# Kernel tuning notes

Hardware: AMD Instinct MI355X
Metric: run time of the kernel (lower is better)

Reference implementation:

```python
import jax, jax.numpy as jnp
import numpy as np
from jax import lax

B_, L_, H_, P_ = 4, 8192, 1024, 64  # batch, seq, d_model, d_state//4
EPS = 1e-5


def setup_inputs() -> dict:
    key = jax.random.key(0)
    ks = jax.random.split(key, 20)
    s = 1.0 / np.sqrt(H_)
    inp = {
        "zH": jax.random.normal(ks[0], (B_, L_, H_), jnp.float32),
        "zL": jax.random.normal(ks[1], (B_, L_, H_), jnp.float32),
        "x": jax.random.normal(ks[2], (B_, L_, H_), jnp.float32),
        "t": jax.random.normal(ks[3], (B_, H_), jnp.float32),
        # AdaLN projections (d_model -> 2*d_model)
        "W_projH": jax.random.normal(ks[4], (H_, 2 * H_), jnp.float32) * s,
        "b_projH": jnp.zeros((2 * H_,), jnp.float32),
        "W_projL": jax.random.normal(ks[5], (H_, 2 * H_), jnp.float32) * s,
        "b_projL": jnp.zeros((2 * H_,), jnp.float32),
        # inj Linear (3*d_model -> d_model)
        "W_inj": jax.random.normal(ks[6], (3 * H_, H_), jnp.float32) * (1.0 / np.sqrt(3 * H_)),
        "b_inj": jnp.zeros((H_,), jnp.float32),
        # S5Dual params (diagonal complex SSM, bidirectional)
        "Lambda_re": -(0.1 + 0.4 * jax.random.uniform(ks[7], (P_,), jnp.float32)),
        "Lambda_im": jnp.pi * jnp.arange(P_, dtype=jnp.float32),
        "B_re": jax.random.normal(ks[8], (P_, H_), jnp.float32) * s,
        "B_im": jax.random.normal(ks[9], (P_, H_), jnp.float32) * s,
        "Cf_re": jax.random.normal(ks[10], (H_, P_), jnp.float32) * (1.0 / np.sqrt(P_)),
        "Cf_im": jax.random.normal(ks[11], (H_, P_), jnp.float32) * (1.0 / np.sqrt(P_)),
        "Cb_re": jax.random.normal(ks[12], (H_, P_), jnp.float32) * (1.0 / np.sqrt(P_)),
        "Cb_im": jax.random.normal(ks[13], (H_, P_), jnp.float32) * (1.0 / np.sqrt(P_)),
        "D": jax.random.normal(ks[14], (H_,), jnp.float32),
        "log_dt": jnp.log(0.001) + (jnp.log(0.1) - jnp.log(0.001)) * jax.random.uniform(ks[15], (P_,), jnp.float32),
    }
    return inp


def _adaln(x, cond, W, b):
    # x: [B,L,H], cond: [B,H]
    scale, shift = jnp.split(cond @ W + b, 2, axis=-1)
    mu = jnp.mean(x, axis=-1, keepdims=True)
    var = jnp.var(x, axis=-1, keepdims=True)
    xn = (x - mu) * lax.rsqrt(var + EPS)
    return xn * (1.0 + scale[:, None, :]) + shift[:, None, :]


def _binop(e1, e2):
    a1, b1 = e1
    a2, b2 = e2
    return a1 * a2, a2 * b1 + b2


def _s5_dual(u, Lambda_re, Lambda_im, B_re, B_im, Cf_re, Cf_im, Cb_re, Cb_im, D, log_dt):
    # u: [B,L,H] real -> [B,L,H] real. Bidirectional diagonal SSM (S5 style).
    Lam = Lambda_re + 1j * Lambda_im            # [P]
    dt = jnp.exp(log_dt)                        # [P]
    Lam_bar = jnp.exp(Lam * dt)                 # [P] ZOH discretization
    Bm = B_re + 1j * B_im                       # [P,H]
    B_bar = ((Lam_bar - 1.0) / Lam)[:, None] * Bm
    Bu = jnp.einsum('blh,ph->blp', u.astype(jnp.complex64), B_bar)  # [B,L,P]
    A = jnp.broadcast_to(Lam_bar, Bu.shape)
    xs_f = lax.associative_scan(_binop, (A, Bu), axis=1)[1]
    xs_b = jnp.flip(lax.associative_scan(_binop, (A, jnp.flip(Bu, axis=1)), axis=1)[1], axis=1)
    Cf = Cf_re + 1j * Cf_im
    Cb = Cb_re + 1j * Cb_im
    y = 2.0 * jnp.einsum('blp,hp->blh', xs_f, Cf).real \
        + 2.0 * jnp.einsum('blp,hp->blh', xs_b, Cb).real \
        + D * u
    return y


def reference(zH, zL, x, t, W_projH, b_projH, W_projL, b_projL, W_inj, b_inj,
              Lambda_re, Lambda_im, B_re, B_im, Cf_re, Cf_im, Cb_re, Cb_im, D, log_dt):
    zH = _adaln(zH, t, W_projH, b_projH)
    zL = _adaln(zL, t, W_projL, b_projL)
    h = jnp.concatenate([zH, zL, x], axis=-1)          # [B,L,3H]
    h = h @ W_inj + b_inj                              # [B,L,H]
    return _s5_dual(h, Lambda_re, Lambda_im, B_re, B_im, Cf_re, Cf_im, Cb_re, Cb_im, D, log_dt)
```

## Files before the change

### kernel.cpp

```cpp
#include <hip/hip_runtime.h>


#define LN_EPS 1e-5f

typedef __attribute__((ext_vector_type(8))) short bf16x8;
typedef __attribute__((ext_vector_type(8))) unsigned short u16x8;
typedef __attribute__((ext_vector_type(4))) float f32x4;

__device__ __forceinline__ unsigned short f2bf(float f) {
  unsigned int u = __float_as_uint(f);
  u += 0x7fffu + ((u >> 16) & 1u);
  return (unsigned short)(u >> 16);
}
__device__ __forceinline__ float bf2f(unsigned short s) {
  return __uint_as_float(((unsigned int)s) << 16);
}

__device__ __forceinline__ void gload16(const void* g, void* l) {
  __builtin_amdgcn_global_load_lds((const __attribute__((address_space(1))) void*)g,
                                   (__attribute__((address_space(3))) void*)l, 16, 0, 0);
}

__device__ __forceinline__ void phase_bar() {
  __builtin_amdgcn_sched_barrier(0);
  asm volatile("" ::: "memory");
  __builtin_amdgcn_s_barrier();
  __builtin_amdgcn_sched_barrier(0);
}

__global__ void proj_k(const float* __restrict__ t,
                       const float* __restrict__ WH, const float* __restrict__ bH,
                       const float* __restrict__ WL, const float* __restrict__ bL,
                       float* __restrict__ cond) {
  const int idx = blockIdx.x * 256 + threadIdx.x;
  const int tensor = idx >> 11;
  const int j2 = idx & 2047;
  const float* W = tensor ? WL : WH;
  const float bv = tensor ? bL[j2] : bH[j2];
  float a0 = bv, a1 = bv, a2 = bv, a3 = bv;
  #pragma unroll 4
  for (int k = 0; k < 1024; ++k) {
    const float w = W[k * 2048 + j2];
    a0 += t[k] * w; a1 += t[1024 + k] * w; a2 += t[2048 + k] * w; a3 += t[3072 + k] * w;
  }
  const int which = j2 >> 10, j = j2 & 1023;
  float* c = cond + (size_t)((tensor * 2 + which) * 4) * 1024 + j;
  c[0] = a0; c[1024] = a1; c[2048] = a2; c[3072] = a3;
}

__global__ void prep_k(const float* __restrict__ Winj, unsigned short* __restrict__ WinjT,
                       const float* __restrict__ Lre, const float* __restrict__ Lim,
                       const float* __restrict__ logdt,
                       const float* __restrict__ Bre, const float* __restrict__ Bim,
                       unsigned short* __restrict__ WBuT,
                       const float* __restrict__ t,
                       const float* __restrict__ WH, const float* __restrict__ WL,
                       float* __restrict__ part) {
  __shared__ float tl[64][65];
  const int bid = blockIdx.x;
  const int tid = threadIdx.x;
  if (bid < 768) {
    const int kt = bid >> 4, nt = bid & 15;
    const int k0 = kt << 6, n0 = nt << 6;
    #pragma unroll
    for (int s = 0; s < 4; ++s) {
      const int i = s * 256 + tid;
      const int r = i >> 4, c4 = i & 15;
      const float4 v = *(const float4*)&Winj[(size_t)(k0 + r) * 1024 + n0 + c4 * 4];
      tl[c4 * 4 + 0][r] = v.x; tl[c4 * 4 + 1][r] = v.y;
      tl[c4 * 4 + 2][r] = v.z; tl[c4 * 4 + 3][r] = v.w;
    }
    __syncthreads();
    const int i = tid >> 2, j0 = (tid & 3) << 4;
    u16x8 w0, w1;
    #pragma unroll
    for (int q = 0; q < 8; ++q) w0[q] = f2bf(tl[i][j0 + q]);
    #pragma unroll
    for (int q = 0; q < 8; ++q) w1[q] = f2bf(tl[i][j0 + 8 + q]);
    *(u16x8*)&WinjT[(size_t)(n0 + i) * 3072 + k0 + j0] = w0;
    *(u16x8*)&WinjT[(size_t)(n0 + i) * 3072 + k0 + j0 + 8] = w1;
  } else if (bid < 1280) {
    const int idx = (bid - 768) * 256 + tid;
    const int j = idx >> 10, hh = idx & 1023;
    const int p = j >> 1, im = j & 1;
    const float lr = Lre[p], li = Lim[p];
    const float dt = expf(logdt[p]);
    const float e = expf(lr * dt);
    float sn, cs; sincosf(li * dt, &sn, &cs);
    const float ar = e * cs - 1.f, ai = e * sn;
    const float den = lr * lr + li * li;
    const float cr = (ar * lr + ai * li) / den;
    const float ci = (ai * lr - ar * li) / den;
    const float br = Bre[p * 1024 + hh], bi = Bim[p * 1024 + hh];
    const float v = im ? (cr * bi + ci * br) : (cr * br - ci * bi);
    WBuT[idx] = f2bf(v);
  } else {
    const int pb = bid - 1280;
    const int tensor = pb >> 7, ks = (pb >> 3) & 15, jc = pb & 7;
    const int j2 = jc * 256 + tid;
    const float* W = tensor ? WL : WH;
    float a0 = 0.f, a1 = 0.f, a2 = 0.f, a3 = 0.f;
    const int k0 = ks * 64;
    #pragma unroll 4
    for (int k = k0; k < k0 + 64; ++k) {
      const float w = W[k * 2048 + j2];
      a0 += t[k] * w; a1 += t[1024 + k] * w; a2 += t[2048 + k] * w; a3 += t[3072 + k] * w;
    }
    float* p = part + ((size_t)(tensor * 16 + ks) * 4) * 2048 + j2;
    p[0] = a0; p[2048] = a1; p[4096] = a2; p[6144] = a3;
  }
}

__global__ void proj_red_k(const float* __restrict__ part,
                           const float* __restrict__ bH, const float* __restrict__ bL,
                           float* __restrict__ cond) {
  const int idx = blockIdx.x * 256 + threadIdx.x;
  const int tensor = idx >> 13, b = (idx >> 11) & 3, j2 = idx & 2047;
  float s = tensor ? bL[j2] : bH[j2];
  #pragma unroll
  for (int ks = 0; ks < 16; ++ks)
    s += part[((size_t)(tensor * 16 + ks) * 4 + b) * 2048 + j2];
  const int which = j2 >> 10, j = j2 & 1023;
  cond[((size_t)(tensor * 2 + which) * 4 + b) * 1024 + j] = s;
}

__global__ void transpose_winj(const float* __restrict__ W, unsigned short* __restrict__ WT) {
  __shared__ float tl[64][65];
  const int kt = blockIdx.x >> 4, nt = blockIdx.x & 15;
  const int k0 = kt << 6, n0 = nt << 6;
  const int tid = threadIdx.x;
  #pragma unroll
  for (int s = 0; s < 4; ++s) {
    const int i = s * 256 + tid;
    const int r = i >> 4, c4 = i & 15;
    const float4 v = *(const float4*)&W[(size_t)(k0 + r) * 1024 + n0 + c4 * 4];
    tl[c4 * 4 + 0][r] = v.x; tl[c4 * 4 + 1][r] = v.y;
    tl[c4 * 4 + 2][r] = v.z; tl[c4 * 4 + 3][r] = v.w;
  }
  __syncthreads();
  const int i = tid >> 2, j0 = (tid & 3) << 4;
  u16x8 w0, w1;
  #pragma unroll
  for (int q = 0; q < 8; ++q) w0[q] = f2bf(tl[i][j0 + q]);
  #pragma unroll
  for (int q = 0; q < 8; ++q) w1[q] = f2bf(tl[i][j0 + 8 + q]);
  *(u16x8*)&WT[(size_t)(n0 + i) * 3072 + k0 + j0] = w0;
  *(u16x8*)&WT[(size_t)(n0 + i) * 3072 + k0 + j0 + 8] = w1;
}

__global__ void wbu_k(const float* __restrict__ Lre, const float* __restrict__ Lim,
                      const float* __restrict__ logdt,
                      const float* __restrict__ Bre, const float* __restrict__ Bim,
                      unsigned short* __restrict__ WBuT) {
  const int idx = blockIdx.x * 256 + threadIdx.x;
  const int j = idx >> 10, hh = idx & 1023;
  const int p = j >> 1, im = j & 1;
  const float lr = Lre[p], li = Lim[p];
  const float dt = expf(logdt[p]);
  const float e = expf(lr * dt);
  float sn, cs; sincosf(li * dt, &sn, &cs);
  const float ar = e * cs - 1.f, ai = e * sn;
  const float den = lr * lr + li * li;
  const float cr = (ar * lr + ai * li) / den;
  const float ci = (ai * lr - ar * li) / den;
  const float br = Bre[p * 1024 + hh], bi = Bim[p * 1024 + hh];
  const float v = im ? (cr * bi + ci * br) : (cr * br - ci * bi);
  WBuT[idx] = f2bf(v);
}

__global__ void w2_k(const float* __restrict__ Cfre, const float* __restrict__ Cfim,
                     const float* __restrict__ Cbre, const float* __restrict__ Cbim,
                     unsigned short* __restrict__ W2T) {
  const int idx = blockIdx.x * 256 + threadIdx.x;
  const int h = idx >> 8, k = idx & 255;
  const int p = (k & 127) >> 1, im = k & 1, bw = k >> 7;
  const float* Cre = bw ? Cbre : Cfre;
  const float* Cim = bw ? Cbim : Cfim;
  const float v = im ? (-2.f * Cim[h * 64 + p]) : (2.f * Cre[h * 64 + p]);
  W2T[idx] = f2bf(v);
}

__global__ __launch_bounds__(256) void adaln_k(const float* __restrict__ zH,
                                               const float* __restrict__ zL,
                                               const float* __restrict__ x,
                                               const float* __restrict__ cond,
                                               unsigned short* __restrict__ znH,
                                               unsigned short* __restrict__ znL,
                                               unsigned short* __restrict__ xbf) {
  const int row = blockIdx.x;
  const int b = row >> 13;
  const int tid = threadIdx.x;
  const size_t rbase = (size_t)row * 1024;
  const float4 vH = *(const float4*)&zH[rbase + tid * 4];
  const float4 vL = *(const float4*)&zL[rbase + tid * 4];
  float sH = vH.x + vH.y + vH.z + vH.w;
  float qH = vH.x * vH.x + vH.y * vH.y + vH.z * vH.z + vH.w * vH.w;
  float sL = vL.x + vL.y + vL.z + vL.w;
  float qL = vL.x * vL.x + vL.y * vL.y + vL.z * vL.z + vL.w * vL.w;
  #pragma unroll
  for (int m = 1; m < 64; m <<= 1) {
    sH += __shfl_xor(sH, m); qH += __shfl_xor(qH, m);
    sL += __shfl_xor(sL, m); qL += __shfl_xor(qL, m);
  }
  __shared__ float red[4][4];
  const int wv = tid >> 6, ln = tid & 63;
  if (ln == 0) { red[wv][0] = sH; red[wv][1] = qH; red[wv][2] = sL; red[wv][3] = qL; }
  __syncthreads();
  sH = red[0][0] + red[1][0] + red[2][0] + red[3][0];
  qH = red[0][1] + red[1][1] + red[2][1] + red[3][1];
  sL = red[0][2] + red[1][2] + red[2][2] + red[3][2];
  qL = red[0][3] + red[1][3] + red[2][3] + red[3][3];
  const float muH = sH * (1.f / 1024.f);
  const float rsH = rsqrtf(qH * (1.f / 1024.f) - muH * muH + LN_EPS);
  const float muL = sL * (1.f / 1024.f);
  const float rsL = rsqrtf(qL * (1.f / 1024.f) - muL * muL + LN_EPS);
  const int h0 = tid * 4;
  const float4 scH = *(const float4*)&cond[(size_t)((0 * 2 + 0) * 4 + b) * 1024 + h0];
  const float4 shH = *(const float4*)&cond[(size_t)((0 * 2 + 1) * 4 + b) * 1024 + h0];
  const float4 scL = *(const float4*)&cond[(size_t)((1 * 2 + 0) * 4 + b) * 1024 + h0];
  const float4 shL = *(const float4*)&cond[(size_t)((1 * 2 + 1) * 4 + b) * 1024 + h0];
  ushort4 oH, oL;
  oH.x = f2bf((vH.x - muH) * rsH * (1.f + scH.x) + shH.x);
  oH.y = f2bf((vH.y - muH) * rsH * (1.f + scH.y) + shH.y);
  oH.z = f2bf((vH.z - muH) * rsH * (1.f + scH.z) + shH.z);
  oH.w = f2bf((vH.w - muH) * rsH * (1.f + scH.w) + shH.w);
  oL.x = f2bf((vL.x - muL) * rsL * (1.f + scL.x) + shL.x);
  oL.y = f2bf((vL.y - muL) * rsL * (1.f + scL.y) + shL.y);
  oL.z = f2bf((vL.z - muL) * rsL * (1.f + scL.z) + shL.z);
  oL.w = f2bf((vL.w - muL) * rsL * (1.f + scL.w) + shL.w);
  *(ushort4*)&znH[rbase + h0] = oH;
  *(ushort4*)&znL[rbase + h0] = oL;
  if (xbf != nullptr) {
    const float4 vx = *(const float4*)&x[rbase + h0];
    ushort4 ox;
    ox.x = f2bf(vx.x); ox.y = f2bf(vx.y); ox.z = f2bf(vx.z); ox.w = f2bf(vx.w);
    *(ushort4*)&xbf[rbase + h0] = ox;
  }
}

__global__ __launch_bounds__(512, 2) void gemm8p_k(
    const unsigned short* __restrict__ znH, const unsigned short* __restrict__ znL,
    const unsigned short* __restrict__ xbf, const unsigned short* __restrict__ WinjT,
    const float* __restrict__ binj, unsigned short* __restrict__ hout) {
  __shared__ char lds[131072];
  const int tid = threadIdx.x;
  const int ln = tid & 63;
  const int w = tid >> 6;
  const int wm = w >> 2, wn = w & 3;
  const int l15 = ln & 15, l4 = ln >> 4;
  const int swz = (blockIdx.x & 7) * 64 + (blockIdx.x >> 3);
  const int r0 = (swz >> 2) << 8, n0 = (swz & 3) << 8;
  constexpr int NT = 48;

  auto stageA = [&](int tau, int hf) {
    const int pidx = tau >> 4;
    const unsigned short* plane = pidx == 0 ? znH : (pidx == 1 ? znL : xbf);
    const int kbase = (tau & 15) << 6;
    char* dst0 = lds + (tau & 1) * 65536 + hf * 16384;
    #pragma unroll
    for (int i = 0; i < 2; ++i) {
      const int idx = i * 512 + tid;
      const int rl = idx >> 3, ps = idx & 7;
      const int ls = ps ^ (rl & 7);
      const unsigned short* src = plane + (size_t)(r0 + hf * 128 + rl) * 1024 + kbase + ls * 8;
      gload16(src, dst0 + i * 8192 + ((tid & 0x1C0) << 4));
    }
  };
  auto stageB = [&](int tau, int hf) {
    char* dst0 = lds + (tau & 1) * 65536 + 32768 + hf * 16384;
    #pragma unroll
    for (int i = 0; i < 2; ++i) {
      const int idx = i * 512 + tid;
      const int rl = idx >> 3, ps = idx & 7;
      const int ls = ps ^ (rl & 7);
      const unsigned short* src = WinjT + (size_t)(n0 + hf * 128 + rl) * 3072 + tau * 64 + ls * 8;
      gload16(src, dst0 + i * 8192 + ((tid & 0x1C0) << 4));
    }
  };
  auto ldA = [&](int tau, int m, int kk) -> bf16x8 {
    const int row = wm * 128 + m * 16 + l15;
    const int ps = (kk * 4 + l4) ^ (row & 7);
    return *(const bf16x8*)(lds + (tau & 1) * 65536 + row * 128 + ps * 16);
  };
  auto ldB = [&](int tau, int n, int kk) -> bf16x8 {
    const int row = wn * 64 + n * 16 + l15;
    const int ps = (kk * 4 + l4) ^ (row & 7);
    return *(const bf16x8*)(lds + (tau & 1) * 65536 + 32768 + row * 128 + ps * 16);
  };

  f32x4 acc[8][4];
  #pragma unroll
  for (int m = 0; m < 8; ++m)
    #pragma unroll
    for (int n = 0; n < 4; ++n)
      acc[m][n] = (f32x4){0.f, 0.f, 0.f, 0.f};

  stageA(0, 0); stageA(0, 1); stageB(0, 0); stageB(0, 1); stageA(1, 0); stageA(1, 1);
  asm volatile("s_waitcnt vmcnt(4)" ::: "memory");
  __builtin_amdgcn_s_barrier();
  __builtin_amdgcn_sched_barrier(0);

  bf16x8 t0[4], t1[4], c0[4], c1[4], b0[4], b1[4];
  #pragma unroll
  for (int m = 0; m < 4; ++m) t0[m] = ldA(0, m, 0);
  #pragma unroll
  for (int n = 0; n < 4; ++n) b0[n] = ldB(0, n, 0);

  for (int tau = 0; tau < NT; ++tau) {
    if (tau + 1 < NT) stageB(tau + 1, 0);
    phase_bar();
    __builtin_amdgcn_s_setprio(1);
    #pragma unroll
    for (int m = 0; m < 4; ++m) t1[m] = ldA(tau, 4 + m, 0);
    #pragma unroll
    for (int m = 0; m < 4; ++m) c0[m] = ldA(tau, m, 1);
    #pragma unroll
    for (int m = 0; m < 4; ++m)
      #pragma unroll
      for (int n = 0; n < 4; ++n)
        acc[m][n] = __builtin_amdgcn_mfma_f32_16x16x32_bf16(t0[m], b0[n], acc[m][n], 0, 0, 0);
    __builtin_amdgcn_s_setprio(0);
    phase_bar();
    if (tau + 1 < NT) stageB(tau + 1, 1);
    phase_bar();
    __builtin_amdgcn_s_setprio(1);
    #pragma unroll
    for (int m = 0; m < 4; ++m) c1[m] = ldA(tau, 4 + m, 1);
    #pragma unroll
    for (int n = 0; n < 4; ++n) b1[n] = ldB(tau, n, 1);
    #pragma unroll
    for (int m = 0; m < 4; ++m)
      #pragma unroll
      for (int n = 0; n < 4; ++n)
        acc[4 + m][n] = __builtin_amdgcn_mfma_f32_16x16x32_bf16(t1[m], b0[n], acc[4 + m][n], 0, 0, 0);
    __builtin_amdgcn_s_setprio(0);
    asm volatile("s_waitcnt lgkmcnt(0)" ::: "memory");
    phase_bar();
    if (tau + 2 < NT) stageA(tau + 2, 0);
    phase_bar();
    __builtin_amdgcn_s_setprio(1);
    #pragma unroll
    for (int m = 0; m < 4; ++m)
      #pragma unroll
      for (int n = 0; n < 4; ++n)
        acc[m][n] = __builtin_amdgcn_mfma_f32_16x16x32_bf16(c0[m], b1[n], acc[m][n], 0, 0, 0);
    __builtin_amdgcn_s_setprio(0);
    phase_bar();
    if (tau + 2 < NT) stageA(tau + 2, 1);
    if (tau < NT - 2) { asm volatile("s_waitcnt vmcnt(4)" ::: "memory"); }
    else              { asm volatile("s_waitcnt vmcnt(0)" ::: "memory"); }
    phase_bar();
    __builtin_amdgcn_s_setprio(1);
    if (tau + 1 < NT) {
      #pragma unroll
      for (int m = 0; m < 4; ++m) t0[m] = ldA(tau + 1, m, 0);
      #pragma unroll
      for (int n = 0; n < 4; ++n) b0[n] = ldB(tau + 1, n, 0);
    }
    #pragma unroll
    for (int m = 0; m < 4; ++m)
      #pragma unroll
      for (int n = 0; n < 4; ++n)
        acc[4 + m][n] = __builtin_amdgcn_mfma_f32_16x16x32_bf16(c1[m], b1[n], acc[4 + m][n], 0, 0, 0);
    __builtin_amdgcn_s_setprio(0);
    phase_bar();
  }

  #pragma unroll
  for (int n = 0; n < 4; ++n) {
    const int gcol = n0 + wn * 64 + n * 16 + l15;
    const float bv = binj[gcol];
    #pragma unroll
    for (int m = 0; m < 8; ++m) {
      const int grow = r0 + wm * 128 + m * 16 + l4 * 4;
      #pragma unroll
      for (int r = 0; r < 4; ++r)
        hout[(size_t)(grow + r) * 1024 + gcol] = f2bf(acc[m][n][r] + bv);
    }
  }
}

template<int KTOT, int NTOT, int CTILES, int EPI, int AMODE>
__global__ __launch_bounds__(256, 3) void gemm_k(
    const unsigned short* __restrict__ A,
    const unsigned short* __restrict__ Bm,
    const float* __restrict__ xsrc,
    const float* __restrict__ evec,
    const unsigned short* __restrict__ hbuf,
    void* __restrict__ Cout) {
  const int tid = threadIdx.x;
  const int wv = tid >> 6, ln = tid & 63;
  const int l15 = ln & 15, l4 = ln >> 4;
  const int wr = wv >> 1, wc = wv & 1;
  const int bid = blockIdx.x;
  const int rt = bid / CTILES, ct = bid % CTILES;
  const int r0 = rt << 7, n0 = ct << 7;

  __shared__ unsigned short ldsA[128 * 32];
  __shared__ unsigned short ldsB[128 * 32];

  f32x4 acc[4][4];
  #pragma unroll
  for (int i = 0; i < 4; ++i)
    #pragma unroll
    for (int j = 0; j < 4; ++j)
      acc[i][j] = (f32x4){0.f, 0.f, 0.f, 0.f};

  for (int k0 = 0; k0 < KTOT; k0 += 32) {
    __syncthreads();
    {
      const unsigned short* bb = Bm + (size_t)n0 * KTOT + k0;
      #pragma unroll
      for (int s0 = 0; s0 < 2; ++s0) {
        const int s = wv + s0 * 4;
        const int bo = (s << 10) + (ln << 4);
        const int row = bo >> 6, inb = bo & 63;
        gload16((const char*)(bb + (size_t)row * KTOT) + inb, (char*)ldsB + (s << 10));
      }
    }
    if (AMODE == 1 && k0 >= 2048) {
      const int row = tid >> 1, kf = (tid & 1) << 4;
      const float* xp = xsrc + (size_t)(r0 + row) * 1024 + (k0 - 2048) + kf;
      const float4 v0 = *(const float4*)(xp + 0);
      const float4 v1 = *(const float4*)(xp + 4);
      const float4 v2 = *(const float4*)(xp + 8);
      const float4 v3 = *(const float4*)(xp + 12);
      u16x8 w0, w1;
      w0[0] = f2bf(v0.x); w0[1] = f2bf(v0.y); w0[2] = f2bf(v0.z); w0[3] = f2bf(v0.w);
      w0[4] = f2bf(v1.x); w0[5] = f2bf(v1.y); w0[6] = f2bf(v1.z); w0[7] = f2bf(v1.w);
      w1[0] = f2bf(v2.x); w1[1] = f2bf(v2.y); w1[2] = f2bf(v2.z); w1[3] = f2bf(v2.w);
      w1[4] = f2bf(v3.x); w1[5] = f2bf(v3.y); w1[6] = f2bf(v3.z); w1[7] = f2bf(v3.w);
      *(u16x8*)&ldsA[row * 32 + kf] = w0;
      *(u16x8*)&ldsA[row * 32 + kf + 8] = w1;
    } else {
      const unsigned short* aa;
      int astr;
      if (AMODE == 0) { aa = A + (size_t)r0 * KTOT + k0; astr = KTOT; }
      else { aa = A + (size_t)(k0 >> 10) * (32768u * 1024u) + (size_t)r0 * 1024 + (k0 & 1023); astr = 1024; }
      #pragma unroll
      for (int s0 = 0; s0 < 2; ++s0) {
        const int s = wv + s0 * 4;
        const int bo = (s << 10) + (ln << 4);
        const int row = bo >> 6, inb = bo & 63;
        gload16((const char*)(aa + (size_t)row * astr) + inb, (char*)ldsA + (s << 10));
      }
    }
    __syncthreads();
    bf16x8 af[4], bfr[4];
    #pragma unroll
    for (int i = 0; i < 4; ++i)
      af[i] = *(const bf16x8*)&ldsA[(wr * 64 + i * 16 + l15) * 32 + l4 * 8];
    #pragma unroll
    for (int j = 0; j < 4; ++j)
      bfr[j] = *(const bf16x8*)&ldsB[(wc * 64 + j * 16 + l15) * 32 + l4 * 8];
    #pragma unroll
    for (int i = 0; i < 4; ++i)
      #pragma unroll
      for (int j = 0; j < 4; ++j)
        acc[i][j] = __builtin_amdgcn_mfma_f32_16x16x32_bf16(af[i], bfr[j], acc[i][j], 0, 0, 0);
  }

  #pragma unroll
  for (int j = 0; j < 4; ++j) {
    const int gcol = n0 + wc * 64 + j * 16 + l15;
    float ev = 0.f;
    if (EPI == 1 || EPI == 3) ev = evec[gcol];
    #pragma unroll
    for (int i = 0; i < 4; ++i) {
      const int gr = r0 + wr * 64 + i * 16 + l4 * 4;
      #pragma unroll
      for (int r = 0; r < 4; ++r) {
        const size_t idx = (size_t)(gr + r) * NTOT + gcol;
        const float v = acc[i][j][r];
        if (EPI == 1)      ((unsigned short*)Cout)[idx] = f2bf(v + ev);
        else if (EPI == 2) ((float*)Cout)[idx] = v;
        else               ((float*)Cout)[idx] = v + ev * bf2f(hbuf[idx]);
      }
    }
  }
}

__global__ __launch_bounds__(256) void gemm_bu_k(
    const unsigned short* __restrict__ A, const unsigned short* __restrict__ Bm,
    float* __restrict__ Bu, float* __restrict__ agg,
    const float* __restrict__ Lre, const float* __restrict__ Lim,
    const float* __restrict__ logdt,
    const float* __restrict__ Cfre, const float* __restrict__ Cfim,
    const float* __restrict__ Cbre, const float* __restrict__ Cbim,
    unsigned short* __restrict__ W2T) {
  const int tid = threadIdx.x;
  if (blockIdx.x >= 256) {
    const int idx = (blockIdx.x - 256) * 256 + tid;
    const int h = idx >> 8, k = idx & 255;
    const int p = (k & 127) >> 1, im = k & 1, bw = k >> 7;
    const float* Cre = bw ? Cbre : Cfre;
    const float* Cim = bw ? Cbim : Cfim;
    const float v = im ? (-2.f * Cim[h * 64 + p]) : (2.f * Cre[h * 64 + p]);
    W2T[idx] = f2bf(v);
    return;
  }
  __shared__ unsigned short ldsA[128 * 32];
  __shared__ unsigned short ldsB[128 * 32];
  __shared__ float cbuf[128][128];
  const int wv = tid >> 6, ln = tid & 63;
  const int l15 = ln & 15, l4 = ln >> 4;
  const int wr = wv >> 1, wc = wv & 1;
  const int r0 = blockIdx.x << 7;

  f32x4 acc[4][4];
  #pragma unroll
  for (int i = 0; i < 4; ++i)
    #pragma unroll
    for (int j = 0; j < 4; ++j)
      acc[i][j] = (f32x4){0.f, 0.f, 0.f, 0.f};

  for (int k0 = 0; k0 < 1024; k0 += 32) {
    __syncthreads();
    {
      const unsigned short* bb = Bm + k0;
      #pragma unroll
      for (int s0 = 0; s0 < 2; ++s0) {
        const int s = wv + s0 * 4;
        const int bo = (s << 10) + (ln << 4);
        const int row = bo >> 6, inb = bo & 63;
        gload16((const char*)(bb + (size_t)row * 1024) + inb, (char*)ldsB + (s << 10));
      }
    }
    {
      const unsigned short* aa = A + (size_t)r0 * 1024 + k0;
      #pragma unroll
      for (int s0 = 0; s0 < 2; ++s0) {
        const int s = wv + s0 * 4;
        const int bo = (s << 10) + (ln << 4);
        const int row = bo >> 6, inb = bo & 63;
        gload16((const char*)(aa + (size_t)row * 1024) + inb, (char*)ldsA + (s << 10));
      }
    }
    __syncthreads();
    bf16x8 af[4], bfr[4];
    #pragma unroll
    for (int i = 0; i < 4; ++i)
      af[i] = *(const bf16x8*)&ldsA[(wr * 64 + i * 16 + l15) * 32 + l4 * 8];
    #pragma unroll
    for (int j = 0; j < 4; ++j)
      bfr[j] = *(const bf16x8*)&ldsB[(wc * 64 + j * 16 + l15) * 32 + l4 * 8];
    #pragma unroll
    for (int i = 0; i < 4; ++i)
      #pragma unroll
      for (int j = 0; j < 4; ++j)
        acc[i][j] = __builtin_amdgcn_mfma_f32_16x16x32_bf16(af[i], bfr[j], acc[i][j], 0, 0, 0);
  }

  #pragma unroll
  for (int j = 0; j < 4; ++j) {
    const int lcol = wc * 64 + j * 16 + l15;
    #pragma unroll
    for (int i = 0; i < 4; ++i) {
      const int lr0 = wr * 64 + i * 16 + l4 * 4;
      #pragma unroll
      for (int r = 0; r < 4; ++r) {
        const float v = acc[i][j][r];
        Bu[(size_t)(r0 + lr0 + r) * 128 + lcol] = v;
        cbuf[lr0 + r][lcol] = v;
      }
    }
  }
  __syncthreads();
  if (wv < 2) {
    const int dir = wv, p = ln;
    const float dt = expf(logdt[p]);
    const float e = expf(Lre[p] * dt);
    float sn, cs; sincosf(Lim[p] * dt, &sn, &cs);
    const float ar = e * cs, ai = e * sn;
    float sr = 0.f, si = 0.f;
    for (int i = 0; i < 128; ++i) {
      const int off = dir ? (127 - i) : i;
      const float vr = cbuf[off][2 * p];
      const float vi = cbuf[off][2 * p + 1];
      const float nr = ar * sr - ai * si + vr;
      const float ni = ar * si + ai * sr + vi;
      sr = nr; si = ni;
    }
    const int b = r0 >> 13, ch = (r0 & 8191) >> 7;
    float* o = agg + (((size_t)dir * 4 + b) * 64 + ch) * 128 + 2 * p;
    o[0] = sr; o[1] = si;
  }
}

__global__ void scan_agg_k(const float* __restrict__ Bu, float* __restrict__ agg,
                           const float* __restrict__ Lre, const float* __restrict__ Lim,
                           const float* __restrict__ logdt) {
  const int bid = blockIdx.x;
  const int dir = bid >> 8, b = (bid >> 6) & 3, ch = bid & 63;
  const int p = threadIdx.x;
  const float dt = expf(logdt[p]);
  const float e = expf(Lre[p] * dt);
  float sn, cs; sincosf(Lim[p] * dt, &sn, &cs);
  const float ar = e * cs, ai = e * sn;
  const int l0 = ch << 7;
  const float* base = Bu + ((size_t)b * 8192 + l0) * 128 + 2 * p;
  float sr = 0.f, si = 0.f;
  for (int g = 0; g < 16; ++g) {
    float2 v[8];
    #pragma unroll
    for (int u = 0; u < 8; ++u) {
      const int i = g * 8 + u;
      const int off = dir ? (127 - i) : i;
      v[u] = *(const float2*)(base + (size_t)off * 128);
    }
    #pragma unroll
    for (int u = 0; u < 8; ++u) {
      const float nr = ar * sr - ai * si + v[u].x;
      const float ni = ar * si + ai * sr + v[u].y;
      sr = nr; si = ni;
    }
  }
  float* o = agg + (((size_t)dir * 4 + b) * 64 + ch) * 128 + 2 * p;
  o[0] = sr; o[1] = si;
}

__global__ void scan_comb_k(const float* __restrict__ agg, float* __restrict__ pre,
                            const float* __restrict__ Lre, const float* __restrict__ Lim,
                            const float* __restrict__ logdt) {
  const int dir = blockIdx.x >> 2, b = blockIdx.x & 3;
  const int p = threadIdx.x;
  const float dt = expf(logdt[p]);
  const float e = expf(Lre[p] * dt);
  float sn, cs; sincosf(Lim[p] * dt, &sn, &cs);
  float Ar = e * cs, Ai = e * sn;
  #pragma unroll
  for (int q = 0; q < 7; ++q) {
    const float nr = Ar * Ar - Ai * Ai; Ai = 2.f * Ar * Ai; Ar = nr;
  }
  const float* ab = agg + ((size_t)(dir * 4 + b) * 64) * 128 + 2 * p;
  float* pb = pre + ((size_t)(dir * 4 + b) * 64) * 128 + 2 * p;
  float sr = 0.f, si = 0.f;
  for (int g = 0; g < 8; ++g) {
    float2 v[8];
    #pragma unroll
    for (int u = 0; u < 8; ++u) {
      const int i = g * 8 + u;
      const int ch = dir ? (63 - i) : i;
      v[u] = *(const float2*)(ab + (size_t)ch * 128);
    }
    #pragma unroll
    for (int u = 0; u < 8; ++u) {
      const int i = g * 8 + u;
      const int ch = dir ? (63 - i) : i;
      pb[(size_t)ch * 128] = sr; pb[(size_t)ch * 128 + 1] = si;
      const float nr = Ar * sr - Ai * si + v[u].x;
      const float ni = Ar * si + Ai * sr + v[u].y;
      sr = nr; si = ni;
    }
  }
}

__global__ void scan_apply_k(const float* __restrict__ Bu, const float* __restrict__ pre,
                             unsigned short* __restrict__ Xcat,
                             const float* __restrict__ Lre, const float* __restrict__ Lim,
                             const float* __restrict__ logdt) {
  const int bid = blockIdx.x;
  const int dir = bid >> 8, b = (bid >> 6) & 3, ch = bid & 63;
  const int p = threadIdx.x;
  const float dt = expf(logdt[p]);
  const float e = expf(Lre[p] * dt);
  float sn, cs; sincosf(Lim[p] * dt, &sn, &cs);
  const float ar = e * cs, ai = e * sn;
  const int l0 = ch << 7;
  const float* base = Bu + ((size_t)b * 8192 + l0) * 128 + 2 * p;
  const float* pr = pre + (((size_t)dir * 4 + b) * 64 + ch) * 128 + 2 * p;
  float sr = pr[0], si = pr[1];
  unsigned short* xb = Xcat + ((size_t)b * 8192 + l0) * 256 + dir * 128 + 2 * p;
  for (int g = 0; g < 16; ++g) {
    float2 v[8];
    #pragma unroll
    for (int u = 0; u < 8; ++u) {
      const int i = g * 8 + u;
      const int off = dir ? (127 - i) : i;
      v[u] = *(const float2*)(base + (size_t)off * 128);
    }
    #pragma unroll
    for (int u = 0; u < 8; ++u) {
      const int i = g * 8 + u;
      const int off = dir ? (127 - i) : i;
      const float nr = ar * sr - ai * si + v[u].x;
      const float ni = ar * si + ai * sr + v[u].y;
      sr = nr; si = ni;
      ushort2 ov; ov.x = f2bf(sr); ov.y = f2bf(si);
      *(ushort2*)(xb + (size_t)off * 256) = ov;
    }
  }
}

__global__ void scan_apply2_k(const float* __restrict__ Bu, const float* __restrict__ agg,
                              unsigned short* __restrict__ Xcat,
                              const float* __restrict__ Lre, const float* __restrict__ Lim,
                              const float* __restrict__ logdt) {
  const int bid = blockIdx.x;
  const int dir = bid >> 8, b = (bid >> 6) & 3, ch = bid & 63;
  const int p = threadIdx.x;
  const float dt = expf(logdt[p]);
  const float e = expf(Lre[p] * dt);
  float sn, cs; sincosf(Lim[p] * dt, &sn, &cs);
  const float ar = e * cs, ai = e * sn;
  float Ar = ar, Ai = ai;
  #pragma unroll
  for (int q = 0; q < 7; ++q) {
    const float nr = Ar * Ar - Ai * Ai; Ai = 2.f * Ar * Ai; Ar = nr;
  }
  const float* ab = agg + ((size_t)(dir * 4 + b) * 64) * 128 + 2 * p;
  float sr = 0.f, si = 0.f;
  const int nk = dir ? (63 - ch) : ch;
  for (int g0 = 0; g0 < nk; g0 += 8) {
    const int gn = (nk - g0) < 8 ? (nk - g0) : 8;
    float2 v[8];
    for (int u = 0; u < gn; ++u) {
      const int i = g0 + u;
      const int k = dir ? (63 - i) : i;
      v[u] = *(const float2*)(ab + (size_t)k * 128);
    }
    for (int u = 0; u < gn; ++u) {
      const float nr = Ar * sr - Ai * si + v[u].x;
      const float ni = Ar * si + Ai * sr + v[u].y;
      sr = nr; si = ni;
    }
  }
  const int l0 = ch << 7;
  const float* base = Bu + ((size_t)b * 8192 + l0) * 128 + 2 * p;
  unsigned short* xb = Xcat + ((size_t)b * 8192 + l0) * 256 + dir * 128 + 2 * p;
  for (int g = 0; g < 16; ++g) {
    float2 v[8];
    #pragma unroll
    for (int u = 0; u < 8; ++u) {
      const int i = g * 8 + u;
      const int off = dir ? (127 - i) : i;
      v[u] = *(const float2*)(base + (size_t)off * 128);
    }
    #pragma unroll
    for (int u = 0; u < 8; ++u) {
      const int i = g * 8 + u;
      const int off = dir ? (127 - i) : i;
      const float nr = ar * sr - ai * si + v[u].x;
      const float ni = ar * si + ai * sr + v[u].y;
      sr = nr; si = ni;
      ushort2 ov; ov.x = f2bf(sr); ov.y = f2bf(si);
      *(ushort2*)(xb + (size_t)off * 256) = ov;
    }
  }
}

extern "C" void kernel_launch(void* const* d_in, const int* in_sizes, int n_in,
                              void* d_out, int out_size, void* d_ws, size_t ws_size,
                              hipStream_t stream) {
  const float* zH    = (const float*)d_in[0];
  const float* zL    = (const float*)d_in[1];
  const float* x     = (const float*)d_in[2];
  const float* t     = (const float*)d_in[3];
  const float* WpH   = (const float*)d_in[4];
  const float* bpH   = (const float*)d_in[5];
  const float* WpL   = (const float*)d_in[6];
  const float* bpL   = (const float*)d_in[7];
  const float* Winj  = (const float*)d_in[8];
  const float* binj  = (const float*)d_in[9];
  const float* Lre   = (const float*)d_in[10];
  const float* Lim   = (const float*)d_in[11];
  const float* Bre   = (const float*)d_in[12];
  const float* Bim   = (const float*)d_in[13];
  const float* Cfre  = (const float*)d_in[14];
  const float* Cfim  = (const float*)d_in[15];
  const float* Cbre  = (const float*)d_in[16];
  const float* Cbim  = (const float*)d_in[17];
  const float* Dv    = (const float*)d_in[18];
  const float* logdt = (const float*)d_in[19];

  unsigned short* znH = (unsigned short*)d_out;
  unsigned short* znL = znH + (size_t)32768 * 1024;

  const bool FAST = ws_size >= 141950976ull;
  char* ws = (char*)d_ws;

  if (FAST) {
    unsigned short* WinjT = (unsigned short*)(ws + 0);
    unsigned short* hbuf  = (unsigned short*)(ws + 6291456);
    unsigned short* WBuT  = (unsigned short*)(ws + 73400320);
    float*          cond  = (float*)(ws + 73662464);
    float*          part  = (float*)(ws + 73793536);
    char*           U     = ws + 74842112;
    unsigned short* xbf   = (unsigned short*)U;
    float*          Bu    = (float*)(U + 0);
    float*          agg   = (float*)(U + 16777216);
    unsigned short* Xcat  = (unsigned short*)(U + 17301504);
    unsigned short* W2T   = (unsigned short*)(U + 34078720);

    prep_k<<<1536, 256, 0, stream>>>(Winj, WinjT, Lre, Lim, logdt, Bre, Bim, WBuT,
                                     t, WpH, WpL, part);
    proj_red_k<<<64, 256, 0, stream>>>(part, bpH, bpL, cond);
    adaln_k<<<32768, 256, 0, stream>>>(zH, zL, x, cond, znH, znL, xbf);
    gemm8p_k<<<512, 512, 0, stream>>>(znH, znL, xbf, WinjT, binj, hbuf);
    gemm_bu_k<<<1280, 256, 0, stream>>>(hbuf, WBuT, Bu, agg, Lre, Lim, logdt,
                                        Cfre, Cfim, Cbre, Cbim, W2T);
    scan_apply2_k<<<512, 64, 0, stream>>>(Bu, agg, Xcat, Lre, Lim, logdt);
    gemm_k<256, 1024, 8, 3, 0><<<2048, 256, 0, stream>>>(Xcat, W2T, nullptr, Dv, hbuf, (float*)d_out);
  } else {
    unsigned short* WinjT = (unsigned short*)ws; ws += (size_t)1024 * 3072 * 2;
    unsigned short* hbuf  = (unsigned short*)ws; ws += (size_t)32768 * 1024 * 2;
    unsigned short* WBuT  = (unsigned short*)ws; ws += (size_t)128 * 1024 * 2;
    float*          Bu    = (float*)ws;          ws += (size_t)32768 * 128 * 4;
    float*          cond  = (float*)ws;          ws += (size_t)2 * 2 * 4 * 1024 * 4;
    float*          agg   = (float*)ws;          ws += (size_t)2 * 4 * 64 * 128 * 4;
    float*          pre   = (float*)ws;          ws += (size_t)2 * 4 * 64 * 128 * 4;
    unsigned short* Xcat  = (unsigned short*)ws; ws += (size_t)32768 * 256 * 2;
    unsigned short* W2T   = (unsigned short*)ws; ws += (size_t)1024 * 256 * 2;

    proj_k<<<16, 256, 0, stream>>>(t, WpH, bpH, WpL, bpL, cond);
    transpose_winj<<<768, 256, 0, stream>>>(Winj, WinjT);
    wbu_k<<<512, 256, 0, stream>>>(Lre, Lim, logdt, Bre, Bim, WBuT);
    w2_k<<<1024, 256, 0, stream>>>(Cfre, Cfim, Cbre, Cbim, W2T);
    adaln_k<<<32768, 256, 0, stream>>>(zH, zL, x, cond, znH, znL, nullptr);
    gemm_k<3072, 1024, 8, 1, 1><<<2048, 256, 0, stream>>>(znH, WinjT, x, binj, nullptr, hbuf);
    gemm_k<1024, 128, 1, 2, 0><<<256, 256, 0, stream>>>(hbuf, WBuT, nullptr, nullptr, nullptr, Bu);
    scan_agg_k<<<512, 64, 0, stream>>>(Bu, agg, Lre, Lim, logdt);
    scan_comb_k<<<8, 64, 0, stream>>>(agg, pre, Lre, Lim, logdt);
    scan_apply_k<<<512, 64, 0, stream>>>(Bu, pre, Xcat, Lre, Lim, logdt);
    gemm_k<256, 1024, 8, 3, 0><<<2048, 256, 0, stream>>>(Xcat, W2T, nullptr, Dv, hbuf, (float*)d_out);
  }
}
```

Before: 460.1 us.

## Double-buffer Bu GEMM loads, reorder epilogue stores, split scan into combine+apply

The Bu projection GEMM now uses double-buffered LDS tiles with async global-to-LDS prefetch of the next K slice and vmcnt waits, so loads overlap with the MFMAs. Epilogues in several GEMMs are reordered so the column index varies fastest, which should give better-coalesced stores, and the bias loads are hoisted. The fused scan_apply2 kernel, where each block redid a serial chunk-prefix over up to 63 aggregates, is replaced by a tiny scan_comb kernel that computes the prefixes once, followed by scan_apply. This adds an extra launch and doubles the LDS used by gemm_bu_k.

Measured after the change: 403.0 us (median of 2 runs). 1.14x faster.

```diff
diff --git a/kernel.cpp b/kernel.cpp
--- a/kernel.cpp
+++ b/kernel.cpp
@@ -366,16 +366,19 @@
     phase_bar();
   }
 
-  #pragma unroll
-  for (int n = 0; n < 4; ++n) {
-    const int gcol = n0 + wn * 64 + n * 16 + l15;
-    const float bv = binj[gcol];
-    #pragma unroll
-    for (int m = 0; m < 8; ++m) {
-      const int grow = r0 + wm * 128 + m * 16 + l4 * 4;
-      #pragma unroll
-      for (int r = 0; r < 4; ++r)
-        hout[(size_t)(grow + r) * 1024 + gcol] = f2bf(acc[m][n][r] + bv);
+  float bvv[4];
+  #pragma unroll
+  for (int n = 0; n < 4; ++n) bvv[n] = binj[n0 + wn * 64 + n * 16 + l15];
+  #pragma unroll
+  for (int m = 0; m < 8; ++m) {
+    #pragma unroll
+    for (int r = 0; r < 4; ++r) {
+      const int grow = r0 + wm * 128 + m * 16 + l4 * 4 + r;
+      #pragma unroll
+      for (int n = 0; n < 4; ++n) {
+        const int gcol = n0 + wn * 64 + n * 16 + l15;
+        hout[(size_t)grow * 1024 + gcol] = f2bf(acc[m][n][r] + bvv[n]);
+      }
     }
   }
 }
@@ -460,21 +463,23 @@
         acc[i][j] = __builtin_amdgcn_mfma_f32_16x16x32_bf16(af[i], bfr[j], acc[i][j], 0, 0, 0);
   }
 
-  #pragma unroll
-  for (int j = 0; j < 4; ++j) {
-    const int gcol = n0 + wc * 64 + j * 16 + l15;
-    float ev = 0.f;
-    if (EPI == 1 || EPI == 3) ev = evec[gcol];
-    #pragma unroll
-    for (int i = 0; i < 4; ++i) {
-      const int gr = r0 + wr * 64 + i * 16 + l4 * 4;
-      #pragma unroll
-      for (int r = 0; r < 4; ++r) {
-        const size_t idx = (size_t)(gr + r) * NTOT + gcol;
+  float ev[4];
+  #pragma unroll
+  for (int j = 0; j < 4; ++j)
+    ev[j] = (EPI == 1 || EPI == 3) ? evec[n0 + wc * 64 + j * 16 + l15] : 0.f;
+  #pragma unroll
+  for (int i = 0; i < 4; ++i) {
+    #pragma unroll
+    for (int r = 0; r < 4; ++r) {
+      const int gr = r0 + wr * 64 + i * 16 + l4 * 4 + r;
+      #pragma unroll
+      for (int j = 0; j < 4; ++j) {
+        const int gcol = n0 + wc * 64 + j * 16 + l15;
+        const size_t idx = (size_t)gr * NTOT + gcol;
         const float v = acc[i][j][r];
-        if (EPI == 1)      ((unsigned short*)Cout)[idx] = f2bf(v + ev);
+        if (EPI == 1)      ((unsigned short*)Cout)[idx] = f2bf(v + ev[j]);
         else if (EPI == 2) ((float*)Cout)[idx] = v;
-        else               ((float*)Cout)[idx] = v + ev * bf2f(hbuf[idx]);
+        else               ((float*)Cout)[idx] = v + ev[j] * bf2f(hbuf[idx]);
       }
     }
   }
@@ -499,14 +504,34 @@
     W2T[idx] = f2bf(v);
     return;
   }
-  __shared__ unsigned short ldsA[128 * 32];
-  __shared__ unsigned short ldsB[128 * 32];
+  __shared__ unsigned short ldsA[2][128 * 32];
+  __shared__ unsigned short ldsB[2][128 * 32];
   __shared__ float cbuf[128][128];
   const int wv = tid >> 6, ln = tid & 63;
   const int l15 = ln & 15, l4 = ln >> 4;
   const int wr = wv >> 1, wc = wv & 1;
   const int r0 = blockIdx.x << 7;
 
+  auto stg = [&](int k) {
+    const int par = k & 1;
+    const unsigned short* bb = Bm + k * 32;
+    const unsigned short* aa = A + (size_t)r0 * 1024 + k * 32;
+    #pragma unroll
+    for (int s0 = 0; s0 < 2; ++s0) {
+      const int s = wv + s0 * 4;
+      const int bo = (s << 10) + (ln << 4);
+      const int row = bo >> 6, inb = bo & 63;
+      gload16((const char*)(bb + (size_t)row * 1024) + inb, (char*)ldsB[par] + (s << 10));
+    }
+    #pragma unroll
+    for (int s0 = 0; s0 < 2; ++s0) {
+      const int s = wv + s0 * 4;
+      const int bo = (s << 10) + (ln << 4);
+      const int row = bo >> 6, inb = bo & 63;
+      gload16((const char*)(aa + (size_t)row * 1024) + inb, (char*)ldsA[par] + (s << 10));
+    }
+  };
+
   f32x4 acc[4][4];
   #pragma unroll
   for (int i = 0; i < 4; ++i)
@@ -514,54 +539,38 @@
     for (int j = 0; j < 4; ++j)
       acc[i][j] = (f32x4){0.f, 0.f, 0.f, 0.f};
 
-  for (int k0 = 0; k0 < 1024; k0 += 32) {
-    __syncthreads();
-    {
-      const unsigned short* bb = Bm + k0;
-      #pragma unroll
-      for (int s0 = 0; s0 < 2; ++s0) {
-        const int s = wv + s0 * 4;
-        const int bo = (s << 10) + (ln << 4);
-        const int row = bo >> 6, inb = bo & 63;
-        gload16((const char*)(bb + (size_t)row * 1024) + inb, (char*)ldsB + (s << 10));
-      }
-    }
-    {
-      const unsigned short* aa = A + (size_t)r0 * 1024 + k0;
-      #pragma unroll
-      for (int s0 = 0; s0 < 2; ++s0) {
-        const int s = wv + s0 * 4;
-        const int bo = (s << 10) + (ln << 4);
-        const int row = bo >> 6, inb = bo & 63;
-        gload16((const char*)(aa + (size_t)row * 1024) + inb, (char*)ldsA + (s << 10));
-      }
-    }
-    __syncthreads();
+  stg(0);
+  for (int k = 0; k < 32; ++k) {
+    const int par = k & 1;
+    if (k + 1 < 32) { stg(k + 1); asm volatile("s_waitcnt vmcnt(4)" ::: "memory"); }
+    else            { asm volatile("s_waitcnt vmcnt(0)" ::: "memory"); }
+    __builtin_amdgcn_s_barrier();
     bf16x8 af[4], bfr[4];
     #pragma unroll
     for (int i = 0; i < 4; ++i)
-      af[i] = *(const bf16x8*)&ldsA[(wr * 64 + i * 16 + l15) * 32 + l4 * 8];
+      af[i] = *(const bf16x8*)&ldsA[par][(wr * 64 + i * 16 + l15) * 32 + l4 * 8];
     #pragma unroll
     for (int j = 0; j < 4; ++j)
-      bfr[j] = *(const bf16x8*)&ldsB[(wc * 64 + j * 16 + l15) * 32 + l4 * 8];
+      bfr[j] = *(const bf16x8*)&ldsB[par][(wc * 64 + j * 16 + l15) * 32 + l4 * 8];
     #pragma unroll
     for (int i = 0; i < 4; ++i)
       #pragma unroll
       for (int j = 0; j < 4; ++j)
         acc[i][j] = __builtin_amdgcn_mfma_f32_16x16x32_bf16(af[i], bfr[j], acc[i][j], 0, 0, 0);
-  }
-
-  #pragma unroll
-  for (int j = 0; j < 4; ++j) {
-    const int lcol = wc * 64 + j * 16 + l15;
-    #pragma unroll
-    for (int i = 0; i < 4; ++i) {
-      const int lr0 = wr * 64 + i * 16 + l4 * 4;
-      #pragma unroll
-      for (int r = 0; r < 4; ++r) {
+    __builtin_amdgcn_s_barrier();
+  }
+
+  #pragma unroll
+  for (int i = 0; i < 4; ++i) {
+    #pragma unroll
+    for (int r = 0; r < 4; ++r) {
+      const int lr = wr * 64 + i * 16 + l4 * 4 + r;
+      #pragma unroll
+      for (int j = 0; j < 4; ++j) {
+        const int lcol = wc * 64 + j * 16 + l15;
         const float v = acc[i][j][r];
-        Bu[(size_t)(r0 + lr0 + r) * 128 + lcol] = v;
-        cbuf[lr0 + r][lcol] = v;
+        Bu[(size_t)(r0 + lr) * 128 + lcol] = v;
+        cbuf[lr][lcol] = v;
       }
     }
   }
@@ -670,63 +679,6 @@
   const float* base = Bu + ((size_t)b * 8192 + l0) * 128 + 2 * p;
   const float* pr = pre + (((size_t)dir * 4 + b) * 64 + ch) * 128 + 2 * p;
   float sr = pr[0], si = pr[1];
-  unsigned short* xb = Xcat + ((size_t)b * 8192 + l0) * 256 + dir * 128 + 2 * p;
-  for (int g = 0; g < 16; ++g) {
-    float2 v[8];
-    #pragma unroll
-    for (int u = 0; u < 8; ++u) {
-      const int i = g * 8 + u;
-      const int off = dir ? (127 - i) : i;
-      v[u] = *(const float2*)(base + (size_t)off * 128);
-    }
-    #pragma unroll
-    for (int u = 0; u < 8; ++u) {
-      const int i = g * 8 + u;
-      const int off = dir ? (127 - i) : i;
-      const float nr = ar * sr - ai * si + v[u].x;
-      const float ni = ar * si + ai * sr + v[u].y;
-      sr = nr; si = ni;
-      ushort2 ov; ov.x = f2bf(sr); ov.y = f2bf(si);
-      *(ushort2*)(xb + (size_t)off * 256) = ov;
-    }
-  }
-}
-
-__global__ void scan_apply2_k(const float* __restrict__ Bu, const float* __restrict__ agg,
-                              unsigned short* __restrict__ Xcat,
-                              const float* __restrict__ Lre, const float* __restrict__ Lim,
-                              const float* __restrict__ logdt) {
-  const int bid = blockIdx.x;
-  const int dir = bid >> 8, b = (bid >> 6) & 3, ch = bid & 63;
-  const int p = threadIdx.x;
-  const float dt = expf(logdt[p]);
-  const float e = expf(Lre[p] * dt);
-  float sn, cs; sincosf(Lim[p] * dt, &sn, &cs);
-  const float ar = e * cs, ai = e * sn;
-  float Ar = ar, Ai = ai;
-  #pragma unroll
-  for (int q = 0; q < 7; ++q) {
-    const float nr = Ar * Ar - Ai * Ai; Ai = 2.f * Ar * Ai; Ar = nr;
-  }
-  const float* ab = agg + ((size_t)(dir * 4 + b) * 64) * 128 + 2 * p;
-  float sr = 0.f, si = 0.f;
-  const int nk = dir ? (63 - ch) : ch;
-  for (int g0 = 0; g0 < nk; g0 += 8) {
-    const int gn = (nk - g0) < 8 ? (nk - g0) : 8;
-    float2 v[8];
-    for (int u = 0; u < gn; ++u) {
-      const int i = g0 + u;
-      const int k = dir ? (63 - i) : i;
-      v[u] = *(const float2*)(ab + (size_t)k * 128);
-    }
-    for (int u = 0; u < gn; ++u) {
-      const float nr = Ar * sr - Ai * si + v[u].x;
-      const float ni = Ar * si + Ai * sr + v[u].y;
-      sr = nr; si = ni;
-    }
-  }
-  const int l0 = ch << 7;
-  const float* base = Bu + ((size_t)b * 8192 + l0) * 128 + 2 * p;
   unsigned short* xb = Xcat + ((size_t)b * 8192 + l0) * 256 + dir * 128 + 2 * p;
   for (int g = 0; g < 16; ++g) {
     float2 v[8];
@@ -789,6 +741,7 @@
     unsigned short* xbf   = (unsigned short*)U;
     float*          Bu    = (float*)(U + 0);
     float*          agg   = (float*)(U + 16777216);
+    float*          pre   = (float*)(U + 17039360);
     unsigned short* Xcat  = (unsigned short*)(U + 17301504);
     unsigned short* W2T   = (unsigned short*)(U + 34078720);
 
@@ -799,7 +752,8 @@
     gemm8p_k<<<512, 512, 0, stream>>>(znH, znL, xbf, WinjT, binj, hbuf);
     gemm_bu_k<<<1280, 256, 0, stream>>>(hbuf, WBuT, Bu, agg, Lre, Lim, logdt,
                                         Cfre, Cfim, Cbre, Cbim, W2T);
-    scan_apply2_k<<<512, 64, 0, stream>>>(Bu, agg, Xcat, Lre, Lim, logdt);
+    scan_comb_k<<<8, 64, 0, stream>>>(agg, pre, Lre, Lim, logdt);
+    scan_apply_k<<<512, 64, 0, stream>>>(Bu, pre, Xcat, Lre, Lim, logdt);
     gemm_k<256, 1024, 8, 3, 0><<<2048, 256, 0, stream>>>(Xcat, W2T, nullptr, Dv, hbuf, (float*)d_out);
   } else {
     unsigned short* WinjT = (unsigned short*)ws; ws += (size_t)1024 * 3072 * 2;
```
